# Optimization experiments

Hardware: AMD Instinct MI355X
Metric: run time of the kernel (lower is better)

Reference implementation:

```python
import jax, jax.numpy as jnp
import numpy as np

N, IN_F, H_F = 200000, 128, 128
INJ, S, E, T = 256, 512, 8192, 32
FEAT_MIN, FEAT_MAX = -1.0, 1.0
NORM_EPS = 1e-8  # torch cosine_similarity eps
SIG_EPS = 1e-9


def _leaky(x):
    return jax.nn.leaky_relu(x, 0.01)


def _gcn(x, src, dst, W, b):
    # PyG GCNConv: add self loops, sym-normalize, aggregate src->dst.
    n = x.shape[0]
    loop = jnp.arange(n, dtype=src.dtype)
    s = jnp.concatenate([src, loop])
    d = jnp.concatenate([dst, loop])
    xw = x @ W  # [n, H]
    deg = jnp.zeros((n,), xw.dtype).at[d].add(jnp.ones((), xw.dtype))
    dinv = jnp.where(deg > 0, jax.lax.rsqrt(deg), 0.0)
    norm = dinv[s] * dinv[d]  # [E+n]
    out = jnp.zeros_like(xw).at[d].add(norm[:, None] * xw[s])
    return out + b


def setup_inputs():
    key = jax.random.key(0)
    ks = jax.random.split(key, 12)
    s1 = 1.0 / np.sqrt(IN_F)
    s2 = 1.0 / np.sqrt(H_F)
    sg = 1.0 / np.sqrt(3 * H_F)
    return {
        "features_tensor": jax.random.normal(ks[0], (N, IN_F), jnp.float32),
        "all_edge_index": jax.random.randint(ks[1], (INJ, 2, E), 0, S, jnp.int32),
        "all_subset": jax.random.randint(ks[2], (INJ, S), 0, N, jnp.int32),
        "remains": jax.random.randint(ks[3], (INJ, T), 0, S, jnp.int32),
        "all_mapping": jax.random.randint(ks[4], (INJ,), 0, S, jnp.int32),
        "inj_num": INJ,
        "W1": jax.random.normal(ks[5], (IN_F, H_F), jnp.float32) * s1,
        "b1": jnp.zeros((H_F,), jnp.float32),
        "W2": jax.random.normal(ks[6], (H_F, H_F), jnp.float32) * s2,
        "b2": jnp.zeros((H_F,), jnp.float32),
        "Wg": jax.random.normal(ks[7], (3 * H_F, 2 * IN_F), jnp.float32) * sg,
        "bg": jnp.zeros((2 * IN_F,), jnp.float32),
        "eps": jax.random.normal(ks[8], (INJ, IN_F), jnp.float32),
    }


def reference(features_tensor, all_edge_index, all_subset, remains, all_mapping,
              inj_num, W1, b1, W2, b2, Wg, bg, eps):
    del inj_num  # implied by leading axis of the batched subgraph tensors
    fs = features_tensor[all_subset]  # [I, S, F] gathered subgraph features
    tgt_feats = jnp.take_along_axis(fs, remains[..., None], axis=1)  # [I, T, F]
    ru_inj = tgt_feats.mean(axis=1)  # [I, F]

    def per_subgraph(x, ei):
        h = _leaky(_gcn(x, ei[0], ei[1], W1, b1))
        h = _leaky(_gcn(h, ei[0], ei[1], W2, b2))
        return h

    h = jax.vmap(per_subgraph)(fs, all_edge_index)  # [I, S, H]
    inj_h = jnp.take_along_axis(h, all_mapping[:, None, None], axis=1)[:, 0]  # [I, H]
    tgt_h = jnp.take_along_axis(h, remains[..., None], axis=1).mean(axis=1)  # [I, H]
    hidden = jnp.concatenate([h.mean(axis=1), inj_h, tgt_h], axis=-1)  # [I, 3H]

    fd = _leaky(hidden @ Wg + bg)  # [I, 2F]
    F_ = features_tensor.shape[1]
    mu = fd[:, :F_]
    sigma = jnp.abs(fd[:, F_:]) + SIG_EPS
    feat = jnp.clip(mu + sigma * eps, FEAT_MIN, FEAT_MAX)  # Normal rsample + clamp

    num = jnp.sum(ru_inj * feat, axis=-1)
    den = (jnp.maximum(jnp.linalg.norm(ru_inj, axis=-1), NORM_EPS)
           * jnp.maximum(jnp.linalg.norm(feat, axis=-1), NORM_EPS))
    homophily = (num / den).mean()
    return feat, mu, sigma, homophily
```

## Files before the change

### kernel.cpp

```cpp
#include <hip/hip_runtime.h>

#define N_NODES 512
#define EDGES   8192
#define TREM    32
#define INJ_N   256

typedef __attribute__((ext_vector_type(2))) float        f32x2;
typedef __attribute__((ext_vector_type(4))) float        f32x4;
typedef __attribute__((ext_vector_type(4))) unsigned int u32x4;
typedef __attribute__((ext_vector_type(8))) __bf16       bf16x8;

static constexpr int OFF_R0   = 0;
static constexpr int OFF_CSR  = 131072;
static constexpr int OFF_OFFS = 147456;
static constexpr int OFF_CUR  = 149520;
static constexpr int OFF_DINV = 151568;
static constexpr int OFF_SUB  = 153616;
static constexpr int OFF_PERM = 155664;
static constexpr int OFF_REM  = 157712;
static constexpr int OFF_RU   = 157840;
static constexpr int OFF_HID  = 158352;
static constexpr int OFF_HIST = 159888;
static constexpr int OFF_MISC = 160400;
static constexpr int OFF_BIAS = 160528;
static constexpr int SMEM_SZ  = 161040;

__device__ __forceinline__ unsigned f2bfu(float f){
  unsigned u = __float_as_uint(f);
  return (u + 0x7fffu + ((u >> 16) & 1u)) >> 16;
}
__device__ __forceinline__ float bflo(unsigned v){ return __uint_as_float(v << 16); }
__device__ __forceinline__ float bfhi(unsigned v){ return __uint_as_float(v & 0xffff0000u); }
__device__ __forceinline__ float leaky(float x){ return x >= 0.f ? x : 0.01f * x; }
__device__ __forceinline__ int runit(int n, int u){ return (n << 8) | (u << 4); }

__global__ void fg_prep(const float* __restrict__ W1, const float* __restrict__ W2,
                        unsigned* __restrict__ wt){
  int L = blockIdx.x;
  const float* W = L ? W2 : W1;
  unsigned* o = wt + L * 8192;
  for (int t = threadIdx.x; t < 2048; t += 256){
    int kk = t >> 9, cb = (t >> 6) & 7, lane = t & 63;
    int l15 = lane & 15, l4 = lane >> 4;
    int kb = kk * 32 + l4 * 8, c = cb * 16 + l15;
    #pragma unroll
    for (int i = 0; i < 4; ++i)
      o[t * 4 + i] = f2bfu(W[(kb + 2 * i) * 128 + c]) |
                     (f2bfu(W[(kb + 2 * i + 1) * 128 + c]) << 16);
  }
}

__device__ __forceinline__ void gemm_rw(char* smem, const unsigned* __restrict__ wt,
                                        f32x4 (&acc)[4][8], int wv, int lane){
  const int l15 = lane & 15, l4 = lane >> 4;
  #pragma unroll
  for (int kk = 0; kk < 4; ++kk){
    bf16x8 a[4];
    #pragma unroll
    for (int rb = 0; rb < 4; ++rb){
      int row = (wv << 6) + (rb << 4) + l15;
      a[rb] = *(const bf16x8*)(smem + runit(row, (kk << 2) + l4));
    }
    #pragma unroll
    for (int cb = 0; cb < 8; ++cb){
      u32x4 bw = *(const u32x4*)(wt + (((kk << 3) + cb) << 8) + (lane << 2));
      bf16x8 b = __builtin_bit_cast(bf16x8, bw);
      #pragma unroll
      for (int rb = 0; rb < 4; ++rb)
        acc[rb][cb] = __builtin_amdgcn_mfma_f32_16x16x32_bf16(a[rb], b, acc[rb][cb], 0, 0, 0);
    }
  }
}

__device__ __forceinline__ void store_rw(char* smem, const f32x4 (&acc)[4][8], int wv, int lane){
  const int l15 = lane & 15, l4 = lane >> 4;
  #pragma unroll
  for (int rb = 0; rb < 4; ++rb)
    #pragma unroll
    for (int cb = 0; cb < 8; ++cb)
      #pragma unroll
      for (int r = 0; r < 4; ++r){
        int row = (wv << 6) + (rb << 4) + (l4 << 2) + r;
        int col = (cb << 4) + l15;
        *(unsigned short*)(smem + ((row << 8) | (col << 1))) = (unsigned short)f2bfu(acc[rb][cb][r]);
      }
}

__device__ __forceinline__ void prop_pass(char* smem, int n, const float* bias_s,
                                          const float* dinv, const unsigned short* csr,
                                          const int* offs, const int (&voff)[16]){
  float dn = dinv[n];
  f32x2 hq[64];
  {
    int base = n << 8;
    #pragma unroll
    for (int t = 0; t < 16; ++t){
      u32x4 v = *(const u32x4*)(smem + base + voff[t]);
      #pragma unroll
      for (int i = 0; i < 4; ++i)
        hq[t * 4 + i] = (f32x2){dn * bflo(v[i]), dn * bfhi(v[i])};
    }
  }
  int e1 = offs[n + 1];
  for (int e = offs[n]; e < e1; ++e){
    int s = csr[e];
    float w = dinv[s];
    int base = s << 8;
    #pragma unroll
    for (int t = 0; t < 16; ++t){
      u32x4 v = *(const u32x4*)(smem + base + voff[t]);
      #pragma unroll
      for (int i = 0; i < 4; ++i){
        hq[t * 4 + i].x += w * bflo(v[i]);
        hq[t * 4 + i].y += w * bfhi(v[i]);
      }
    }
  }
  __syncthreads();
  int base = n << 8;
  #pragma unroll
  for (int t = 0; t < 16; ++t){
    const float* bp = bias_s + (voff[t] >> 1);
    f32x4 ba = *(const f32x4*)bp;
    f32x4 bb = *(const f32x4*)(bp + 4);
    u32x4 o;
    o[0] = f2bfu(leaky(dn * hq[t*4+0].x + ba.x)) | (f2bfu(leaky(dn * hq[t*4+0].y + ba.y)) << 16);
    o[1] = f2bfu(leaky(dn * hq[t*4+1].x + ba.z)) | (f2bfu(leaky(dn * hq[t*4+1].y + ba.w)) << 16);
    o[2] = f2bfu(leaky(dn * hq[t*4+2].x + bb.x)) | (f2bfu(leaky(dn * hq[t*4+2].y + bb.y)) << 16);
    o[3] = f2bfu(leaky(dn * hq[t*4+3].x + bb.z)) | (f2bfu(leaky(dn * hq[t*4+3].y + bb.w)) << 16);
    *(u32x4*)(smem + base + voff[t]) = o;
  }
  __syncthreads();
}

__global__ __launch_bounds__(512, 2) void fg_main(
    const float* __restrict__ feats, const int* __restrict__ ei_g,
    const int* __restrict__ subset_g, const int* __restrict__ rem_g,
    const int* __restrict__ map_g,
    const float* __restrict__ b1, const float* __restrict__ b2,
    const float* __restrict__ Wg, const float* __restrict__ bg,
    const float* __restrict__ eps_g,
    const unsigned* __restrict__ wt,
    float* __restrict__ out, float* __restrict__ ws_f)
{
  extern __shared__ __align__(16) char smem[];
  const int inj = blockIdx.x;
  const int tid = threadIdx.x;
  const int lane = tid & 63, wv = tid >> 6;

  unsigned short* csr  = (unsigned short*)(smem + OFF_CSR);
  int*   offs   = (int*)  (smem + OFF_OFFS);
  int*   cur    = (int*)  (smem + OFF_CUR);
  float* dinv   = (float*)(smem + OFF_DINV);
  int*   sub    = (int*)  (smem + OFF_SUB);
  int*   perm   = (int*)  (smem + OFF_PERM);
  int*   rem    = (int*)  (smem + OFF_REM);
  float* ru     = (float*)(smem + OFF_RU);
  float* hid    = (float*)(smem + OFF_HID);
  int*   hist   = (int*)  (smem + OFF_HIST);
  int*   histcur= (int*)  (smem + OFF_HIST + 256);
  int*   misc   = (int*)  (smem + OFF_MISC);
  float* redf   = (float*)(smem + OFF_MISC + 64);
  float* bias_s = (float*)(smem + OFF_BIAS);

  int voff[16];
  #pragma unroll
  for (int t = 0; t < 16; ++t) voff[t] = (((lane + t) & 15) << 4);

  sub[tid] = subset_g[inj * N_NODES + tid];
  if (tid < TREM) rem[tid] = rem_g[inj * TREM + tid];
  if (tid == 0) misc[0] = map_g[inj];
  cur[tid] = 0;
  if (tid < 64) hist[tid] = 0;
  __syncthreads();

  const int* ei = ei_g + inj * 2 * EDGES;
  int4 es[4], ed[4];
  #pragma unroll
  for (int k = 0; k < 4; ++k){
    es[k] = *(const int4*)(ei + (tid << 4) + (k << 2));
    ed[k] = *(const int4*)(ei + EDGES + (tid << 4) + (k << 2));
  }
  #pragma unroll
  for (int k = 0; k < 4; ++k){
    atomicAdd(&cur[ed[k].x], 1); atomicAdd(&cur[ed[k].y], 1);
    atomicAdd(&cur[ed[k].z], 1); atomicAdd(&cur[ed[k].w], 1);
  }
  __syncthreads();

  int myc = cur[tid];
  dinv[tid] = 1.0f / sqrtf((float)(myc + 1));
  int v = myc;
  #pragma unroll
  for (int o = 1; o < 64; o <<= 1){
    int t2 = __shfl_up(v, o);
    if (lane >= o) v += t2;
  }
  if (lane == 63) misc[1 + wv] = v;
  atomicAdd(&hist[myc < 63 ? myc : 63], 1);
  __syncthreads();

  int base = 0;
  for (int i = 0; i < wv; ++i) base += misc[1 + i];
  int excl = base + v - myc;
  offs[tid] = excl;
  cur[tid]  = excl;
  if (tid == 0) offs[N_NODES] = EDGES;
  if (tid < 64){
    int hv = hist[tid], sv = hv;
    #pragma unroll
    for (int o = 1; o < 64; o <<= 1){
      int t2 = __shfl_up(sv, o);
      if (tid >= o) sv += t2;
    }
    histcur[tid] = sv - hv;
  }
  __syncthreads();

  #pragma unroll
  for (int k = 0; k < 4; ++k){
    int pos;
    pos = atomicAdd(&cur[ed[k].x], 1); csr[pos] = (unsigned short)es[k].x;
    pos = atomicAdd(&cur[ed[k].y], 1); csr[pos] = (unsigned short)es[k].y;
    pos = atomicAdd(&cur[ed[k].z], 1); csr[pos] = (unsigned short)es[k].z;
    pos = atomicAdd(&cur[ed[k].w], 1); csr[pos] = (unsigned short)es[k].w;
  }
  {
    int rank = atomicAdd(&histcur[myc < 63 ? myc : 63], 1);
    perm[rank] = tid;
  }
  if (tid < 128){
    float s = 0.f;
    for (int j = 0; j < TREM; ++j)
      s += feats[(long)sub[rem[j]] * 128 + tid];
    ru[tid] = s * (1.f / 32.f);
  }
  if (tid >= 384) bias_s[tid & 127] = b1[tid & 127];
  {
    const float* frow = feats + (long)sub[tid] * 128;
    #pragma unroll
    for (int t = 0; t < 16; ++t){
      const float* p = frow + (voff[t] >> 1);
      f32x4 a = *(const f32x4*)p;
      f32x4 b = *(const f32x4*)(p + 4);
      u32x4 pk;
      pk[0] = f2bfu(a.x) | (f2bfu(a.y) << 16);
      pk[1] = f2bfu(a.z) | (f2bfu(a.w) << 16);
      pk[2] = f2bfu(b.x) | (f2bfu(b.y) << 16);
      pk[3] = f2bfu(b.z) | (f2bfu(b.w) << 16);
      *(u32x4*)(smem + (tid << 8) + voff[t]) = pk;
    }
  }
  __syncthreads();

  f32x4 acc[4][8];
  #pragma unroll
  for (int i = 0; i < 4; ++i)
    #pragma unroll
    for (int j = 0; j < 8; ++j) acc[i][j] = (f32x4){0.f, 0.f, 0.f, 0.f};
  gemm_rw(smem, wt, acc, wv, lane);
  __syncthreads();
  store_rw(smem, acc, wv, lane);
  __syncthreads();
  prop_pass(smem, perm[tid], bias_s, dinv, csr, offs, voff);

  if (tid < 128) bias_s[tid] = b2[tid];
  #pragma unroll
  for (int i = 0; i < 4; ++i)
    #pragma unroll
    for (int j = 0; j < 8; ++j) acc[i][j] = (f32x4){0.f, 0.f, 0.f, 0.f};
  gemm_rw(smem, wt + 8192, acc, wv, lane);
  __syncthreads();
  store_rw(smem, acc, wv, lane);
  __syncthreads();
  prop_pass(smem, perm[tid], bias_s, dinv, csr, offs, voff);

  cur[tid] = 0;
  __syncthreads();
  if (tid < TREM) atomicAdd(&cur[rem[tid]], 1);
  __syncthreads();

  float* psum  = (float*)(smem + OFF_CSR);
  float* pwsum = (float*)(smem + OFF_CSR + 4096);
  {
    int cp = tid & 63, ch = tid >> 6;
    int c0 = cp * 2;
    int u = c0 >> 3, bo = (c0 & 7) << 1;
    float s0 = 0, s1 = 0, w0 = 0, w1 = 0;
    for (int k = 0; k < 64; ++k){
      int n = (ch << 6) + k;
      unsigned vv = *(const unsigned*)(smem + ((n << 8) | (u << 4) | bo));
      float lo = bflo(vv), hi = bfhi(vv);
      float wtt = (float)cur[n];
      s0 += lo; s1 += hi;
      w0 += wtt * lo; w1 += wtt * hi;
    }
    psum [ch * 128 + c0] = s0;  psum [ch * 128 + c0 + 1] = s1;
    pwsum[ch * 128 + c0] = w0;  pwsum[ch * 128 + c0 + 1] = w1;
  }
  if (tid < 64){
    int mapn = misc[0];
    int c0 = tid * 2, u = c0 >> 3, bo = (c0 & 7) << 1;
    unsigned vv = *(const unsigned*)(smem + ((mapn << 8) | (u << 4) | bo));
    hid[128 + c0] = bflo(vv); hid[128 + c0 + 1] = bfhi(vv);
  }
  __syncthreads();
  if (tid < 128){
    float s = 0.f, t = 0.f;
    #pragma unroll
    for (int ch = 0; ch < 8; ++ch){ s += psum[ch * 128 + tid]; t += pwsum[ch * 128 + tid]; }
    hid[tid]       = s * (1.f / 512.f);
    hid[256 + tid] = t * (1.f / 32.f);
  }
  __syncthreads();

  float* wgp = (float*)(smem + OFF_CSR);
  {
    int g = tid >> 7, c = tid & 127;
    float f0 = 0.f, f1 = 0.f;
    const float* wb = Wg + (g * 96) * 256;
    #pragma unroll 8
    for (int j = 0; j < 96; ++j){
      float hj = hid[g * 96 + j];
      f0 += hj * wb[j * 256 + c];
      f1 += hj * wb[j * 256 + 128 + c];
    }
    wgp[g * 256 + c]       = f0;
    wgp[g * 256 + 128 + c] = f1;
  }
  __syncthreads();
  if (tid < 128){
    float f0 = bg[tid], f1 = bg[128 + tid];
    #pragma unroll
    for (int g = 0; g < 4; ++g){
      f0 += wgp[g * 256 + tid];
      f1 += wgp[g * 256 + 128 + tid];
    }
    f0 = leaky(f0); f1 = leaky(f1);
    float mu = f0;
    float sg = fabsf(f1) + 1e-9f;
    float ep = eps_g[inj * 128 + tid];
    float ft = fminf(fmaxf(mu + sg * ep, -1.f), 1.f);
    out[         inj * 128 + tid] = ft;
    out[32768 +  inj * 128 + tid] = mu;
    out[65536 +  inj * 128 + tid] = sg;
    float r = ru[tid];
    float pn = r * ft, pr = r * r, pf = ft * ft;
    #pragma unroll
    for (int o = 32; o > 0; o >>= 1){
      pn += __shfl_down(pn, o);
      pr += __shfl_down(pr, o);
      pf += __shfl_down(pf, o);
    }
    if (lane == 0){ redf[wv * 3 + 0] = pn; redf[wv * 3 + 1] = pr; redf[wv * 3 + 2] = pf; }
  }
  __syncthreads();
  if (tid == 0){
    float num = redf[0] + redf[3];
    float r2  = redf[1] + redf[4];
    float f2  = redf[2] + redf[5];
    float den = fmaxf(sqrtf(r2), 1e-8f) * fmaxf(sqrtf(f2), 1e-8f);
    ws_f[inj] = num / den;
  }
}

__global__ void fg_reduce(const float* __restrict__ ws_f, float* __restrict__ out){
  int t = threadIdx.x;
  float v = ws_f[t];
  #pragma unroll
  for (int o = 32; o > 0; o >>= 1) v += __shfl_down(v, o);
  __shared__ float tmp[4];
  if ((t & 63) == 0) tmp[t >> 6] = v;
  __syncthreads();
  if (t == 0) out[98304] = (tmp[0] + tmp[1] + tmp[2] + tmp[3]) * (1.f / 256.f);
}

extern "C" void kernel_launch(void* const* d_in, const int* in_sizes, int n_in,
                              void* d_out, int out_size, void* d_ws, size_t ws_size,
                              hipStream_t stream){
  (void)in_sizes; (void)n_in; (void)out_size; (void)ws_size;
  const float* feats = (const float*)d_in[0];
  const int*   ei    = (const int*)  d_in[1];
  const int*   sub   = (const int*)  d_in[2];
  const int*   rem   = (const int*)  d_in[3];
  const int*   map   = (const int*)  d_in[4];
  const float* W1    = (const float*)d_in[6];
  const float* b1    = (const float*)d_in[7];
  const float* W2    = (const float*)d_in[8];
  const float* b2    = (const float*)d_in[9];
  const float* Wg    = (const float*)d_in[10];
  const float* bg    = (const float*)d_in[11];
  const float* eps   = (const float*)d_in[12];
  float* out = (float*)d_out;
  unsigned* wt = (unsigned*)d_ws;
  float* ws_f  = (float*)((char*)d_ws + 65536);

  fg_prep<<<2, 256, 0, stream>>>(W1, W2, wt);

  hipFuncSetAttribute(reinterpret_cast<const void*>(fg_main),
                      hipFuncAttributeMaxDynamicSharedMemorySize, SMEM_SZ);
  fg_main<<<INJ_N, 512, SMEM_SZ, stream>>>(feats, ei, sub, rem, map,
                                           b1, b2, Wg, bg, eps, wt, out, ws_f);
  fg_reduce<<<1, 256, 0, stream>>>(ws_f, out);
}
```

Before: 279.1 us.

## Double block size to 1024 threads, splitting each node's columns across two halves

The main kernel now launches 1024 threads per subgraph instead of 512. In the propagation pass each node's 128 feature columns are split between two thread halves, and in the GEMM each wave owns 32 rows instead of 64, which halves per-thread accumulator registers. The edge-gather loop now prefetches the next neighbour index and weight one iteration ahead, and the weight-prep kernel is spread over 8 blocks instead of 2. The aim is more latency hiding through more waves per block, at the cost of more synchronisation participants, idle threads in the 512-wide phases, and duplicated CSR index reads per node.

```diff
diff --git a/kernel.cpp b/kernel.cpp
--- a/kernel.cpp
+++ b/kernel.cpp
@@ -36,10 +36,10 @@
 
 __global__ void fg_prep(const float* __restrict__ W1, const float* __restrict__ W2,
                         unsigned* __restrict__ wt){
-  int L = blockIdx.x;
+  int L = blockIdx.x >> 2, q = blockIdx.x & 3;
   const float* W = L ? W2 : W1;
   unsigned* o = wt + L * 8192;
-  for (int t = threadIdx.x; t < 2048; t += 256){
+  for (int t = q * 512 + threadIdx.x; t < q * 512 + 512; t += 256){
     int kk = t >> 9, cb = (t >> 6) & 7, lane = t & 63;
     int l15 = lane & 15, l4 = lane >> 4;
     int kb = kk * 32 + l4 * 8, c = cb * 16 + l15;
@@ -51,14 +51,14 @@
 }
 
 __device__ __forceinline__ void gemm_rw(char* smem, const unsigned* __restrict__ wt,
-                                        f32x4 (&acc)[4][8], int wv, int lane){
+                                        f32x4 (&acc)[2][8], int wv, int lane){
   const int l15 = lane & 15, l4 = lane >> 4;
   #pragma unroll
   for (int kk = 0; kk < 4; ++kk){
-    bf16x8 a[4];
-    #pragma unroll
-    for (int rb = 0; rb < 4; ++rb){
-      int row = (wv << 6) + (rb << 4) + l15;
+    bf16x8 a[2];
+    #pragma unroll
+    for (int rb = 0; rb < 2; ++rb){
+      int row = (wv << 5) + (rb << 4) + l15;
       a[rb] = *(const bf16x8*)(smem + runit(row, (kk << 2) + l4));
     }
     #pragma unroll
@@ -66,21 +66,21 @@
       u32x4 bw = *(const u32x4*)(wt + (((kk << 3) + cb) << 8) + (lane << 2));
       bf16x8 b = __builtin_bit_cast(bf16x8, bw);
       #pragma unroll
-      for (int rb = 0; rb < 4; ++rb)
+      for (int rb = 0; rb < 2; ++rb)
         acc[rb][cb] = __builtin_amdgcn_mfma_f32_16x16x32_bf16(a[rb], b, acc[rb][cb], 0, 0, 0);
     }
   }
 }
 
-__device__ __forceinline__ void store_rw(char* smem, const f32x4 (&acc)[4][8], int wv, int lane){
+__device__ __forceinline__ void store_rw(char* smem, const f32x4 (&acc)[2][8], int wv, int lane){
   const int l15 = lane & 15, l4 = lane >> 4;
   #pragma unroll
-  for (int rb = 0; rb < 4; ++rb)
+  for (int rb = 0; rb < 2; ++rb)
     #pragma unroll
     for (int cb = 0; cb < 8; ++cb)
       #pragma unroll
       for (int r = 0; r < 4; ++r){
-        int row = (wv << 6) + (rb << 4) + (l4 << 2) + r;
+        int row = (wv << 5) + (rb << 4) + (l4 << 2) + r;
         int col = (cb << 4) + l15;
         *(unsigned short*)(smem + ((row << 8) | (col << 1))) = (unsigned short)f2bfu(acc[rb][cb][r]);
       }
@@ -88,38 +88,41 @@
 
 __device__ __forceinline__ void prop_pass(char* smem, int n, const float* bias_s,
                                           const float* dinv, const unsigned short* csr,
-                                          const int* offs, const int (&voff)[16]){
+                                          const int* offs, const int (&voff)[8]){
   float dn = dinv[n];
-  f32x2 hq[64];
+  f32x2 hq[32];
   {
     int base = n << 8;
     #pragma unroll
-    for (int t = 0; t < 16; ++t){
+    for (int t = 0; t < 8; ++t){
       u32x4 v = *(const u32x4*)(smem + base + voff[t]);
       #pragma unroll
       for (int i = 0; i < 4; ++i)
         hq[t * 4 + i] = (f32x2){dn * bflo(v[i]), dn * bfhi(v[i])};
     }
   }
-  int e1 = offs[n + 1];
-  for (int e = offs[n]; e < e1; ++e){
-    int s = csr[e];
-    float w = dinv[s];
-    int base = s << 8;
-    #pragma unroll
-    for (int t = 0; t < 16; ++t){
+  int e0 = offs[n], e1 = offs[n + 1];
+  int s = (e0 < e1) ? csr[e0] : 0;
+  float w = dinv[s];
+  for (int e = e0; e < e1; ){
+    int   base = s << 8;
+    float wc   = w;
+    ++e;
+    if (e < e1){ s = csr[e]; w = dinv[s]; }
+    #pragma unroll
+    for (int t = 0; t < 8; ++t){
       u32x4 v = *(const u32x4*)(smem + base + voff[t]);
       #pragma unroll
       for (int i = 0; i < 4; ++i){
-        hq[t * 4 + i].x += w * bflo(v[i]);
-        hq[t * 4 + i].y += w * bfhi(v[i]);
+        hq[t * 4 + i].x += wc * bflo(v[i]);
+        hq[t * 4 + i].y += wc * bfhi(v[i]);
       }
     }
   }
   __syncthreads();
   int base = n << 8;
   #pragma unroll
-  for (int t = 0; t < 16; ++t){
+  for (int t = 0; t < 8; ++t){
     const float* bp = bias_s + (voff[t] >> 1);
     f32x4 ba = *(const f32x4*)bp;
     f32x4 bb = *(const f32x4*)(bp + 4);
@@ -133,7 +136,7 @@
   __syncthreads();
 }
 
-__global__ __launch_bounds__(512, 2) void fg_main(
+__global__ __launch_bounds__(1024, 4) void fg_main(
     const float* __restrict__ feats, const int* __restrict__ ei_g,
     const int* __restrict__ subset_g, const int* __restrict__ rem_g,
     const int* __restrict__ map_g,
@@ -163,49 +166,55 @@
   float* redf   = (float*)(smem + OFF_MISC + 64);
   float* bias_s = (float*)(smem + OFF_BIAS);
 
-  int voff[16];
-  #pragma unroll
-  for (int t = 0; t < 16; ++t) voff[t] = (((lane + t) & 15) << 4);
-
-  sub[tid] = subset_g[inj * N_NODES + tid];
+  const int half = tid >> 9;
+  int voff[8];
+  #pragma unroll
+  for (int t = 0; t < 8; ++t) voff[t] = (((half << 3) | ((lane + t) & 7)) << 4);
+
+  if (tid < N_NODES) sub[tid] = subset_g[inj * N_NODES + tid];
   if (tid < TREM) rem[tid] = rem_g[inj * TREM + tid];
   if (tid == 0) misc[0] = map_g[inj];
-  cur[tid] = 0;
+  if (tid < N_NODES) cur[tid] = 0;
   if (tid < 64) hist[tid] = 0;
   __syncthreads();
 
   const int* ei = ei_g + inj * 2 * EDGES;
-  int4 es[4], ed[4];
-  #pragma unroll
-  for (int k = 0; k < 4; ++k){
-    es[k] = *(const int4*)(ei + (tid << 4) + (k << 2));
-    ed[k] = *(const int4*)(ei + EDGES + (tid << 4) + (k << 2));
-  }
-  #pragma unroll
-  for (int k = 0; k < 4; ++k){
+  int4 es[2], ed[2];
+  #pragma unroll
+  for (int k = 0; k < 2; ++k){
+    es[k] = *(const int4*)(ei + (tid << 3) + (k << 2));
+    ed[k] = *(const int4*)(ei + EDGES + (tid << 3) + (k << 2));
+  }
+  #pragma unroll
+  for (int k = 0; k < 2; ++k){
     atomicAdd(&cur[ed[k].x], 1); atomicAdd(&cur[ed[k].y], 1);
     atomicAdd(&cur[ed[k].z], 1); atomicAdd(&cur[ed[k].w], 1);
   }
   __syncthreads();
 
-  int myc = cur[tid];
-  dinv[tid] = 1.0f / sqrtf((float)(myc + 1));
-  int v = myc;
-  #pragma unroll
-  for (int o = 1; o < 64; o <<= 1){
-    int t2 = __shfl_up(v, o);
-    if (lane >= o) v += t2;
-  }
-  if (lane == 63) misc[1 + wv] = v;
-  atomicAdd(&hist[myc < 63 ? myc : 63], 1);
-  __syncthreads();
-
-  int base = 0;
-  for (int i = 0; i < wv; ++i) base += misc[1 + i];
-  int excl = base + v - myc;
-  offs[tid] = excl;
-  cur[tid]  = excl;
-  if (tid == 0) offs[N_NODES] = EDGES;
+  int myc = 0, v = 0;
+  if (tid < N_NODES){
+    myc = cur[tid];
+    dinv[tid] = 1.0f / sqrtf((float)(myc + 1));
+    v = myc;
+    #pragma unroll
+    for (int o = 1; o < 64; o <<= 1){
+      int t2 = __shfl_up(v, o);
+      if (lane >= o) v += t2;
+    }
+    if (lane == 63) misc[1 + wv] = v;
+    atomicAdd(&hist[myc < 63 ? myc : 63], 1);
+  }
+  __syncthreads();
+
+  if (tid < N_NODES){
+    int base = 0;
+    for (int i = 0; i < wv; ++i) base += misc[1 + i];
+    int excl = base + v - myc;
+    offs[tid] = excl;
+    cur[tid]  = excl;
+    if (tid == 0) offs[N_NODES] = EDGES;
+  }
   if (tid < 64){
     int hv = hist[tid], sv = hv;
     #pragma unroll
@@ -218,14 +227,14 @@
   __syncthreads();
 
   #pragma unroll
-  for (int k = 0; k < 4; ++k){
+  for (int k = 0; k < 2; ++k){
     int pos;
     pos = atomicAdd(&cur[ed[k].x], 1); csr[pos] = (unsigned short)es[k].x;
     pos = atomicAdd(&cur[ed[k].y], 1); csr[pos] = (unsigned short)es[k].y;
     pos = atomicAdd(&cur[ed[k].z], 1); csr[pos] = (unsigned short)es[k].z;
     pos = atomicAdd(&cur[ed[k].w], 1); csr[pos] = (unsigned short)es[k].w;
   }
-  {
+  if (tid < N_NODES){
     int rank = atomicAdd(&histcur[myc < 63 ? myc : 63], 1);
     perm[rank] = tid;
   }
@@ -235,11 +244,12 @@
       s += feats[(long)sub[rem[j]] * 128 + tid];
     ru[tid] = s * (1.f / 32.f);
   }
-  if (tid >= 384) bias_s[tid & 127] = b1[tid & 127];
+  if (tid >= 896) bias_s[tid & 127] = b1[tid & 127];
   {
-    const float* frow = feats + (long)sub[tid] * 128;
-    #pragma unroll
-    for (int t = 0; t < 16; ++t){
+    int node = tid & 511;
+    const float* frow = feats + (long)sub[node] * 128;
+    #pragma unroll
+    for (int t = 0; t < 8; ++t){
       const float* p = frow + (voff[t] >> 1);
       f32x4 a = *(const f32x4*)p;
       f32x4 b = *(const f32x4*)(p + 4);
@@ -248,47 +258,49 @@
       pk[1] = f2bfu(a.z) | (f2bfu(a.w) << 16);
       pk[2] = f2bfu(b.x) | (f2bfu(b.y) << 16);
       pk[3] = f2bfu(b.z) | (f2bfu(b.w) << 16);
-      *(u32x4*)(smem + (tid << 8) + voff[t]) = pk;
-    }
-  }
-  __syncthreads();
-
-  f32x4 acc[4][8];
-  #pragma unroll
-  for (int i = 0; i < 4; ++i)
+      *(u32x4*)(smem + (node << 8) + voff[t]) = pk;
+    }
+  }
+  __syncthreads();
+
+  const int pnode_i = ((wv & 7) << 6) | lane;
+
+  f32x4 acc[2][8];
+  #pragma unroll
+  for (int i = 0; i < 2; ++i)
     #pragma unroll
     for (int j = 0; j < 8; ++j) acc[i][j] = (f32x4){0.f, 0.f, 0.f, 0.f};
   gemm_rw(smem, wt, acc, wv, lane);
   __syncthreads();
   store_rw(smem, acc, wv, lane);
   __syncthreads();
-  prop_pass(smem, perm[tid], bias_s, dinv, csr, offs, voff);
+  prop_pass(smem, perm[pnode_i], bias_s, dinv, csr, offs, voff);
 
   if (tid < 128) bias_s[tid] = b2[tid];
   #pragma unroll
-  for (int i = 0; i < 4; ++i)
+  for (int i = 0; i < 2; ++i)
     #pragma unroll
     for (int j = 0; j < 8; ++j) acc[i][j] = (f32x4){0.f, 0.f, 0.f, 0.f};
   gemm_rw(smem, wt + 8192, acc, wv, lane);
   __syncthreads();
   store_rw(smem, acc, wv, lane);
   __syncthreads();
-  prop_pass(smem, perm[tid], bias_s, dinv, csr, offs, voff);
-
-  cur[tid] = 0;
+  prop_pass(smem, perm[pnode_i], bias_s, dinv, csr, offs, voff);
+
+  if (tid < N_NODES) cur[tid] = 0;
   __syncthreads();
   if (tid < TREM) atomicAdd(&cur[rem[tid]], 1);
   __syncthreads();
 
   float* psum  = (float*)(smem + OFF_CSR);
-  float* pwsum = (float*)(smem + OFF_CSR + 4096);
+  float* pwsum = (float*)(smem + OFF_CSR + 8192);
   {
     int cp = tid & 63, ch = tid >> 6;
     int c0 = cp * 2;
     int u = c0 >> 3, bo = (c0 & 7) << 1;
     float s0 = 0, s1 = 0, w0 = 0, w1 = 0;
-    for (int k = 0; k < 64; ++k){
-      int n = (ch << 6) + k;
+    for (int k = 0; k < 32; ++k){
+      int n = (ch << 5) + k;
       unsigned vv = *(const unsigned*)(smem + ((n << 8) | (u << 4) | bo));
       float lo = bflo(vv), hi = bfhi(vv);
       float wtt = (float)cur[n];
@@ -308,7 +320,7 @@
   if (tid < 128){
     float s = 0.f, t = 0.f;
     #pragma unroll
-    for (int ch = 0; ch < 8; ++ch){ s += psum[ch * 128 + tid]; t += pwsum[ch * 128 + tid]; }
+    for (int ch = 0; ch < 16; ++ch){ s += psum[ch * 128 + tid]; t += pwsum[ch * 128 + tid]; }
     hid[tid]       = s * (1.f / 512.f);
     hid[256 + tid] = t * (1.f / 32.f);
   }
@@ -318,10 +330,10 @@
   {
     int g = tid >> 7, c = tid & 127;
     float f0 = 0.f, f1 = 0.f;
-    const float* wb = Wg + (g * 96) * 256;
+    const float* wb = Wg + (g * 48) * 256;
     #pragma unroll 8
-    for (int j = 0; j < 96; ++j){
-      float hj = hid[g * 96 + j];
+    for (int j = 0; j < 48; ++j){
+      float hj = hid[g * 48 + j];
       f0 += hj * wb[j * 256 + c];
       f1 += hj * wb[j * 256 + 128 + c];
     }
@@ -332,7 +344,7 @@
   if (tid < 128){
     float f0 = bg[tid], f1 = bg[128 + tid];
     #pragma unroll
-    for (int g = 0; g < 4; ++g){
+    for (int g = 0; g < 8; ++g){
       f0 += wgp[g * 256 + tid];
       f1 += wgp[g * 256 + 128 + tid];
     }
@@ -395,11 +407,11 @@
   unsigned* wt = (unsigned*)d_ws;
   float* ws_f  = (float*)((char*)d_ws + 65536);
 
-  fg_prep<<<2, 256, 0, stream>>>(W1, W2, wt);
+  fg_prep<<<8, 256, 0, stream>>>(W1, W2, wt);
 
   hipFuncSetAttribute(reinterpret_cast<const void*>(fg_main),
                       hipFuncAttributeMaxDynamicSharedMemorySize, SMEM_SZ);
-  fg_main<<<INJ_N, 512, SMEM_SZ, stream>>>(feats, ei, sub, rem, map,
-                                           b1, b2, Wg, bg, eps, wt, out, ws_f);
+  fg_main<<<INJ_N, 1024, SMEM_SZ, stream>>>(feats, ei, sub, rem, map,
+                                            b1, b2, Wg, bg, eps, wt, out, ws_f);
   fg_reduce<<<1, 256, 0, stream>>>(ws_f, out);
 }
```

New measurement: 266.2 us. 4.6% less time.
